# Kernel optimization log

Measured on AMD Instinct MI355X. Metric: run time of the kernel, lower is better.

## Reference

```python
import jax, jax.numpy as jnp
import numpy as np

IN_FEATURES = 256
OUT_FEATURES = 256
INTERNAL = (IN_FEATURES + OUT_FEATURES) // 2  # trajectron AdditiveAttention default


def setup_inputs() -> dict:
    key = jax.random.key(0)
    k1, k2, k3, k4, k5 = jax.random.split(key, 5)
    B, TH, TQ = 32, 256, 64
    inputs = jax.random.normal(k1, (B, TH, IN_FEATURES), dtype=jnp.float32)
    state = jax.random.normal(k2, (B, TQ, OUT_FEATURES), dtype=jnp.float32)
    # Linear weights (no bias), Kaiming-ish scale
    w1 = jax.random.normal(k3, (INTERNAL, IN_FEATURES), dtype=jnp.float32) / np.sqrt(IN_FEATURES)
    w2 = jax.random.normal(k4, (INTERNAL, OUT_FEATURES), dtype=jnp.float32) / np.sqrt(OUT_FEATURES)
    v = jax.random.normal(k5, (INTERNAL,), dtype=jnp.float32) / np.sqrt(INTERNAL)
    return {"inputs": inputs, "state": state, "w1": w1, "w2": w2, "v": v, "batch_size": B}


def reference(inputs, state, w1, w2, v, batch_size):
    # history annotations: (B, Th, Din); future annotations (queries): (B, Tq, Dout)
    keys = inputs.reshape(batch_size, -1, IN_FEATURES)
    queries = state.reshape(batch_size, -1, OUT_FEATURES)
    # Additive (Bahdanau) attention: score = v . tanh(W1 k + W2 q)
    k_proj = jnp.einsum('bti,di->btd', keys, w1)       # (B, Th, D)
    q_proj = jnp.einsum('bqo,do->bqd', queries, w2)    # (B, Tq, D)
    scores = jnp.einsum('d,bqtd->bqt', v, jnp.tanh(q_proj[:, :, None, :] + k_proj[:, None, :, :]))
    alpha = jax.nn.softmax(scores, axis=-1)            # softmax over history axis
    contexts = jnp.einsum('bqt,bti->bqi', alpha, keys)  # (B, Tq, Din)
    # reshape + dropout (eval mode / p effectively 0 -> identity)
    return contexts.reshape(-1, IN_FEATURES)
```

## Files before the change

kernel.cpp:

```cpp
#include <hip/hip_runtime.h>
#include <math.h>

#define BATCH 32
#define TH    256
#define TQn   64
#define DIN   256
#define DD    256
#define QT    4
#define E2C   2.885390081777927f
#define NL2E  -2.8853900817779268f

typedef __attribute__((ext_vector_type(8)))  short bf16x8;
typedef __attribute__((ext_vector_type(16))) float floatx16;
typedef __attribute__((ext_vector_type(4)))  float f32x4;
typedef __attribute__((ext_vector_type(2)))  float f32x2;

__device__ __forceinline__ float eclamp(float x) {
    return __builtin_amdgcn_exp2f(fminf(x * E2C, 15.f));
}

__device__ __forceinline__ f32x2 pk_fma_s(f32x2 a, f32x2 b, f32x2 c) {
    f32x2 d;
    asm("v_pk_fma_f32 %0, %1, %2, %3" : "=v"(d) : "s"(a), "v"(b), "v"(c));
    return d;
}
__device__ __forceinline__ f32x2 pk_mul_s(f32x2 a, f32x2 b) {
    f32x2 d;
    asm("v_pk_mul_f32 %0, %1, %2" : "=v"(d) : "s"(a), "v"(b));
    return d;
}
__device__ __forceinline__ f32x2 pk_mul_v(f32x2 a, f32x2 b) {
    f32x2 d;
    asm("v_pk_mul_f32 %0, %1, %2" : "=v"(d) : "v"(a), "v"(b));
    return d;
}

__device__ __forceinline__ unsigned cvt_pk_bf16(float x0, float x1) {
    unsigned r;
    asm("v_cvt_pk_bf16_f32 %0, %1, %2" : "=v"(r) : "v"(x0), "v"(x1));
    return r;
}
__device__ __forceinline__ void split2(float x0, float x1, unsigned& hi, unsigned& lo) {
    unsigned h = cvt_pk_bf16(x0, x1);
    float f0 = __uint_as_float(h << 16);
    float f1 = __uint_as_float(h & 0xFFFF0000u);
    hi = h;
    lo = cvt_pk_bf16(x0 - f0, x1 - f1);
}

__device__ __forceinline__ void split8(float4 f0, float4 f1, uint4& hi, uint4& lo) {
    split2(f0.x, f0.y, hi.x, lo.x);
    split2(f0.z, f0.w, hi.y, lo.y);
    split2(f1.x, f1.y, hi.z, lo.z);
    split2(f1.z, f1.w, hi.w, lo.w);
}

#define REG4  65
#define WOFF  (16 * REG4)
#define TSTR  68
__global__ __launch_bounds__(256, 4)
void proj_kernel(const float* __restrict__ keys,
                 const float* __restrict__ state,
                 const float* __restrict__ w1,
                 const float* __restrict__ w2,
                 const float* __restrict__ vvec,
                 float* __restrict__ ktp,
                 float* __restrict__ qpo,
                 float* __restrict__ vperm)
{
    __shared__ uint4 lds4[2 * 16 * REG4];

    const int bid = blockIdx.x;
    const int tid = threadIdx.x;

    const float* X;
    const float* W;
    int m0, n0;
    bool is_kp;
    if (bid < 512) {
        is_kp = true;
        m0 = (bid >> 2) * 64;
        n0 = (bid & 3) * 64;
        X = keys; W = w1;
    } else {
        is_kp = false;
        int lb = bid - 512;
        m0 = (lb >> 2) * 64;
        n0 = (lb & 3) * 64;
        X = state; W = w2;
    }

    const int w    = tid >> 6;
    const int l    = tid & 63;
    const int mt   = w >> 1;
    const int nt   = w & 1;
    const int srow = tid >> 3;
    const int kg   = tid & 7;
    const int s_s  = kg >> 1;
    const int lidx = (srow & 31) + 32 * (kg & 1);

    floatx16 acc = {};

    #pragma unroll
    for (int k0 = 0; k0 < DIN; k0 += 64) {
        #pragma unroll
        for (int hrow = 0; hrow < 2; hrow++) {
            int m = srow + hrow * 32;
            const float* px = X + (size_t)(m0 + m) * DIN + k0 + kg * 8;
            uint4 hi, lo;
            split8(*(const float4*)px, *(const float4*)(px + 4), hi, lo);
            int g = m >> 5;
            lds4[((0 * 2 + g) * 4 + s_s) * REG4 + lidx] = hi;
            lds4[((2 + g) * 4 + s_s) * REG4 + lidx] = lo;
            const float* pw = W + (size_t)(n0 + m) * DIN + k0 + kg * 8;
            split8(*(const float4*)pw, *(const float4*)(pw + 4), hi, lo);
            lds4[WOFF + ((0 * 2 + g) * 4 + s_s) * REG4 + lidx] = hi;
            lds4[WOFF + ((2 + g) * 4 + s_s) * REG4 + lidx] = lo;
        }
        __syncthreads();

        #pragma unroll
        for (int s = 0; s < 4; s++) {
            uint4 ahr = lds4[((0 * 2 + mt) * 4 + s) * REG4 + l];
            uint4 alr = lds4[((2 + mt) * 4 + s) * REG4 + l];
            uint4 bhr = lds4[WOFF + ((0 * 2 + nt) * 4 + s) * REG4 + l];
            uint4 blr = lds4[WOFF + ((2 + nt) * 4 + s) * REG4 + l];
            bf16x8 ah = __builtin_bit_cast(bf16x8, ahr);
            bf16x8 al = __builtin_bit_cast(bf16x8, alr);
            bf16x8 bh = __builtin_bit_cast(bf16x8, bhr);
            bf16x8 bl = __builtin_bit_cast(bf16x8, blr);
            acc = __builtin_amdgcn_mfma_f32_32x32x16_bf16(ah, bh, acc, 0, 0, 0);
            acc = __builtin_amdgcn_mfma_f32_32x32x16_bf16(al, bh, acc, 0, 0, 0);
            acc = __builtin_amdgcn_mfma_f32_32x32x16_bf16(ah, bl, acc, 0, 0, 0);
        }
        __syncthreads();
    }

    const int col = l & 31;
    const int hl  = l >> 5;
    if (is_kp) {
        float* sT = (float*)lds4;
        const int d_local = nt * 32 + col;
        #pragma unroll
        for (int r = 0; r < 16; r++) {
            int t_local = mt * 32 + 4 * hl + 8 * (r >> 2) + (r & 3);
            sT[t_local * TSTR + d_local] = eclamp(acc[r]);
        }
        __syncthreads();
        const int b  = m0 >> 8;
        const int t0 = m0 & 255;
        float4* dst4 = (float4*)ktp;
        #pragma unroll
        for (int p = 0; p < 4; p++) {
            int dp_local = w * 4 + p;
            float4 v4 = *(float4*)&sT[l * TSTR + dp_local * 4];
            float4 w4;
            w4.x = v4.x; w4.y = v4.z; w4.z = v4.y; w4.w = v4.w;
            dst4[(size_t)(b * 64 + (n0 >> 2) + dp_local) * 256 + t0 + l] = w4;
        }
    } else {
        const int d  = n0 + nt * 32 + col;
        const int dl = d & 3;
        const int dsd = (d & ~3) | ((dl & 1) << 1) | (dl >> 1);
        #pragma unroll
        for (int r = 0; r < 16; r++) {
            int row = (r & 3) + 8 * (r >> 2) + 4 * hl;
            qpo[(size_t)(m0 + mt * 32 + row) * DD + dsd] = eclamp(acc[r]);
        }
        if (bid == 512 && tid < 256) {
            int jl = tid & 3;
            vperm[tid] = vvec[(tid & ~3) | ((jl & 1) << 1) | (jl >> 1)];
        }
    }
}

__global__ __launch_bounds__(1024, 8)
void attn_kernel(const float* __restrict__ keys,
                 const float* __restrict__ vvec,
                 const float* __restrict__ ktp,
                 const float* __restrict__ qp,
                 float* __restrict__ out)
{
    __shared__ float s_part[4][QT][TH];
    __shared__ float s_alpha[QT][TH];
    __shared__ float s_rsum[QT];

    const int bid  = blockIdx.x;
    const int b    = bid & 31;
    const int q0   = (bid >> 5) * QT;
    const int tid  = threadIdx.x;
    const int t    = tid & 255;
    const int dgu  = __builtin_amdgcn_readfirstlane(tid >> 8);
    const int lane = tid & 63;
    const int wv   = tid >> 6;

    float acc[QT];
    #pragma unroll
    for (int q = 0; q < QT; q++) acc[q] = 0.f;

    const float4* kb4 = (const float4*)ktp + ((size_t)(b * 64 + dgu * 16) * 256 + t);
    const float* pqr0 = qp + (size_t)(b * TQn + q0 + 0) * DD + dgu * 64;
    const float* pqr1 = qp + (size_t)(b * TQn + q0 + 1) * DD + dgu * 64;
    const float* pqr2 = qp + (size_t)(b * TQn + q0 + 2) * DD + dgu * 64;
    const float* pqr3 = qp + (size_t)(b * TQn + q0 + 3) * DD + dgu * 64;
    const float* vvp  = vvec + dgu * 64;

    const f32x2 one2 = {1.f, 1.f};

    float4 kv0 = kb4[0 * 256], kv1 = kb4[1 * 256],
           kv2 = kb4[2 * 256], kv3 = kb4[3 * 256];

    #pragma unroll
    for (int c = 0; c < 4; c++) {
        float4 n0v, n1v, n2v, n3v;
        if (c < 3) {
            const float4* p = kb4 + (size_t)(c + 1) * 4 * 256;
            n0v = p[0 * 256]; n1v = p[1 * 256];
            n2v = p[2 * 256]; n3v = p[3 * 256];
        }
        #pragma unroll
        for (int u = 0; u < 4; u++) {
            const int dp = c * 4 + u;
            float4 kv = (u == 0) ? kv0 : (u == 1) ? kv1 : (u == 2) ? kv2 : kv3;
            f32x2 KA = {kv.x, kv.y};
            f32x2 KB = {kv.z, kv.w};
            f32x4 V4 = *(const f32x4*)(vvp + dp * 4);
            f32x2 VA = {V4[0], V4[1]};
            f32x2 VB = {V4[2], V4[3]};
            const float* pqr[QT] = {pqr0, pqr1, pqr2, pqr3};
            #pragma unroll
            for (int q = 0; q < QT; q++) {
                const float* pr = pqr[q];
                f32x4 P4 = *(const f32x4*)(pr + dp * 4);
                f32x2 PA = {P4[0], P4[1]};
                f32x2 PB = {P4[2], P4[3]};
                f32x2 A = pk_fma_s(PA, KA, one2);
                f32x2 B = pk_fma_s(PB, KB, one2);
                f32x2 D = pk_mul_v(A, B);
                f32x2 T = pk_mul_s(VA, B);
                f32x2 N = pk_fma_s(VB, A, T);
                float num = fmaf(N[1], D[0], N[0] * D[1]);
                float den = D[0] * D[1];
                acc[q] = fmaf(num, __builtin_amdgcn_rcpf(den), acc[q]);
            }
        }
        if (c < 3) { kv0 = n0v; kv1 = n1v; kv2 = n2v; kv3 = n3v; }
    }

    #pragma unroll
    for (int q = 0; q < QT; q++) s_part[dgu][q][t] = acc[q];
    __syncthreads();

    if (wv < QT) {
        const int q = wv;
        float p0 = s_part[0][q][lane]       + s_part[1][q][lane]
                 + s_part[2][q][lane]       + s_part[3][q][lane];
        float p1 = s_part[0][q][lane + 64]  + s_part[1][q][lane + 64]
                 + s_part[2][q][lane + 64]  + s_part[3][q][lane + 64];
        float p2 = s_part[0][q][lane + 128] + s_part[1][q][lane + 128]
                 + s_part[2][q][lane + 128] + s_part[3][q][lane + 128];
        float p3 = s_part[0][q][lane + 192] + s_part[1][q][lane + 192]
                 + s_part[2][q][lane + 192] + s_part[3][q][lane + 192];
        float e0 = __builtin_amdgcn_exp2f(p0 * NL2E);
        float e1 = __builtin_amdgcn_exp2f(p1 * NL2E);
        float e2 = __builtin_amdgcn_exp2f(p2 * NL2E);
        float e3 = __builtin_amdgcn_exp2f(p3 * NL2E);
        s_alpha[q][lane]       = e0;
        s_alpha[q][lane + 64]  = e1;
        s_alpha[q][lane + 128] = e2;
        s_alpha[q][lane + 192] = e3;
        float s = (e0 + e1) + (e2 + e3);
        #pragma unroll
        for (int off = 32; off >= 1; off >>= 1) s += __shfl_xor(s, off);
        if (lane == 0) s_rsum[q] = 1.f / s;
    }
    __syncthreads();

    {
        const int iqg = __builtin_amdgcn_readfirstlane((tid >> 6) & 3);
        const int il  = lane & 15;
        const int tl  = lane >> 4;
        const int iq  = iqg * 16 + il;

        f32x4 ctx4[QT] = {};
        const float* kp0 = keys + ((size_t)b * TH + dgu * 64 + tl) * DIN + iq * 4;

        #pragma unroll 4
        for (int step = 0; step < 16; step++) {
            f32x4 key4 = *(const f32x4*)(kp0 + (size_t)step * 4 * DIN);
            const int ta = dgu * 64 + step * 4 + tl;
            #pragma unroll
            for (int q = 0; q < QT; q++)
                ctx4[q] += key4 * s_alpha[q][ta];
        }

        #pragma unroll
        for (int q = 0; q < QT; q++) {
            #pragma unroll
            for (int k = 0; k < 4; k++) {
                ctx4[q][k] += __shfl_xor(ctx4[q][k], 16);
                ctx4[q][k] += __shfl_xor(ctx4[q][k], 32);
            }
        }
        if (tl == 0) {
            #pragma unroll
            for (int q = 0; q < QT; q++)
                *(f32x4*)&s_part[dgu][q][iq * 4] = ctx4[q];
        }
    }
    __syncthreads();

    if (tid < 256) {
        const int q = tid >> 6, iqf = tid & 63;
        f32x4 s = *(const f32x4*)&s_part[0][q][iqf * 4];
        s += *(const f32x4*)&s_part[1][q][iqf * 4];
        s += *(const f32x4*)&s_part[2][q][iqf * 4];
        s += *(const f32x4*)&s_part[3][q][iqf * 4];
        s *= s_rsum[q];
        *(f32x4*)&out[(size_t)(b * TQn + q0 + q) * DIN + iqf * 4] = s;
    }
}

extern "C" void kernel_launch(void* const* d_in, const int* in_sizes, int n_in,
                              void* d_out, int out_size, void* d_ws, size_t ws_size,
                              hipStream_t stream) {
    (void)in_sizes; (void)n_in; (void)out_size; (void)ws_size;
    const float* keys  = (const float*)d_in[0];
    const float* state = (const float*)d_in[1];
    const float* w1    = (const float*)d_in[2];
    const float* w2    = (const float*)d_in[3];
    const float* v     = (const float*)d_in[4];
    float* out = (float*)d_out;

    float* ktp = (float*)d_ws;
    float* qp  = ktp + (size_t)BATCH * DD * TH;
    float* vp  = qp + (size_t)BATCH * TQn * DD;

    hipLaunchKernelGGL(proj_kernel, dim3(640), dim3(256), 0, stream,
                       keys, state, w1, w2, v, ktp, qp, vp);
    hipLaunchKernelGGL(attn_kernel, dim3(BATCH * (TQn / QT)), dim3(1024), 0, stream,
                       keys, vp, ktp, qp, out);
}
```

Measured before the change: 101.7 us.

## Double queries per attention block, halve block size, transpose alpha for packed context FMA

```diff
diff --git a/kernel.cpp b/kernel.cpp
--- a/kernel.cpp
+++ b/kernel.cpp
@@ -6,9 +6,10 @@
 #define TQn   64
 #define DIN   256
 #define DD    256
-#define QT    4
+#define QT    8
 #define E2C   2.885390081777927f
 #define NL2E  -2.8853900817779268f
+#define ASTR  12
 
 typedef __attribute__((ext_vector_type(8)))  short bf16x8;
 typedef __attribute__((ext_vector_type(16))) float floatx16;
@@ -22,6 +23,11 @@
 __device__ __forceinline__ f32x2 pk_fma_s(f32x2 a, f32x2 b, f32x2 c) {
     f32x2 d;
     asm("v_pk_fma_f32 %0, %1, %2, %3" : "=v"(d) : "s"(a), "v"(b), "v"(c));
+    return d;
+}
+__device__ __forceinline__ f32x2 pk_fma_v(f32x2 a, f32x2 b, f32x2 c) {
+    f32x2 d;
+    asm("v_pk_fma_f32 %0, %1, %2, %3" : "=v"(d) : "v"(a), "v"(b), "v"(c));
     return d;
 }
 __device__ __forceinline__ f32x2 pk_mul_s(f32x2 a, f32x2 b) {
@@ -174,15 +180,15 @@
     }
 }
 
-__global__ __launch_bounds__(1024, 8)
+__global__ __launch_bounds__(512, 4)
 void attn_kernel(const float* __restrict__ keys,
                  const float* __restrict__ vvec,
                  const float* __restrict__ ktp,
                  const float* __restrict__ qp,
                  float* __restrict__ out)
 {
-    __shared__ float s_part[4][QT][TH];
-    __shared__ float s_alpha[QT][TH];
+    __shared__ float s_part[2][QT][TH];
+    __shared__ float s_alphaT[TH][ASTR];
     __shared__ float s_rsum[QT];
 
     const int bid  = blockIdx.x;
@@ -198,12 +204,9 @@
     #pragma unroll
     for (int q = 0; q < QT; q++) acc[q] = 0.f;
 
-    const float4* kb4 = (const float4*)ktp + ((size_t)(b * 64 + dgu * 16) * 256 + t);
-    const float* pqr0 = qp + (size_t)(b * TQn + q0 + 0) * DD + dgu * 64;
-    const float* pqr1 = qp + (size_t)(b * TQn + q0 + 1) * DD + dgu * 64;
-    const float* pqr2 = qp + (size_t)(b * TQn + q0 + 2) * DD + dgu * 64;
-    const float* pqr3 = qp + (size_t)(b * TQn + q0 + 3) * DD + dgu * 64;
-    const float* vvp  = vvec + dgu * 64;
+    const float4* kb4 = (const float4*)ktp + ((size_t)(b * 64 + dgu * 32) * 256 + t);
+    const float* pqb  = qp + (size_t)(b * TQn + q0) * DD + dgu * 128;
+    const float* vvp  = vvec + dgu * 128;
 
     const f32x2 one2 = {1.f, 1.f};
 
@@ -211,9 +214,9 @@
            kv2 = kb4[2 * 256], kv3 = kb4[3 * 256];
 
     #pragma unroll
-    for (int c = 0; c < 4; c++) {
+    for (int c = 0; c < 8; c++) {
         float4 n0v, n1v, n2v, n3v;
-        if (c < 3) {
+        if (c < 7) {
             const float4* p = kb4 + (size_t)(c + 1) * 4 * 256;
             n0v = p[0 * 256]; n1v = p[1 * 256];
             n2v = p[2 * 256]; n3v = p[3 * 256];
@@ -227,11 +230,9 @@
             f32x4 V4 = *(const f32x4*)(vvp + dp * 4);
             f32x2 VA = {V4[0], V4[1]};
             f32x2 VB = {V4[2], V4[3]};
-            const float* pqr[QT] = {pqr0, pqr1, pqr2, pqr3};
             #pragma unroll
             for (int q = 0; q < QT; q++) {
-                const float* pr = pqr[q];
-                f32x4 P4 = *(const f32x4*)(pr + dp * 4);
+                f32x4 P4 = *(const f32x4*)(pqb + q * DD + dp * 4);
                 f32x2 PA = {P4[0], P4[1]};
                 f32x2 PB = {P4[2], P4[3]};
                 f32x2 A = pk_fma_s(PA, KA, one2);
@@ -244,31 +245,27 @@
                 acc[q] = fmaf(num, __builtin_amdgcn_rcpf(den), acc[q]);
             }
         }
-        if (c < 3) { kv0 = n0v; kv1 = n1v; kv2 = n2v; kv3 = n3v; }
+        if (c < 7) { kv0 = n0v; kv1 = n1v; kv2 = n2v; kv3 = n3v; }
     }
 
     #pragma unroll
     for (int q = 0; q < QT; q++) s_part[dgu][q][t] = acc[q];
     __syncthreads();
 
-    if (wv < QT) {
+    {
         const int q = wv;
-        float p0 = s_part[0][q][lane]       + s_part[1][q][lane]
-                 + s_part[2][q][lane]       + s_part[3][q][lane];
-        float p1 = s_part[0][q][lane + 64]  + s_part[1][q][lane + 64]
-                 + s_part[2][q][lane + 64]  + s_part[3][q][lane + 64];
-        float p2 = s_part[0][q][lane + 128] + s_part[1][q][lane + 128]
-                 + s_part[2][q][lane + 128] + s_part[3][q][lane + 128];
-        float p3 = s_part[0][q][lane + 192] + s_part[1][q][lane + 192]
-                 + s_part[2][q][lane + 192] + s_part[3][q][lane + 192];
+        float p0 = s_part[0][q][lane]       + s_part[1][q][lane];
+        float p1 = s_part[0][q][lane + 64]  + s_part[1][q][lane + 64];
+        float p2 = s_part[0][q][lane + 128] + s_part[1][q][lane + 128];
+        float p3 = s_part[0][q][lane + 192] + s_part[1][q][lane + 192];
         float e0 = __builtin_amdgcn_exp2f(p0 * NL2E);
         float e1 = __builtin_amdgcn_exp2f(p1 * NL2E);
         float e2 = __builtin_amdgcn_exp2f(p2 * NL2E);
         float e3 = __builtin_amdgcn_exp2f(p3 * NL2E);
-        s_alpha[q][lane]       = e0;
-        s_alpha[q][lane + 64]  = e1;
-        s_alpha[q][lane + 128] = e2;
-        s_alpha[q][lane + 192] = e3;
+        s_alphaT[lane][q]       = e0;
+        s_alphaT[lane + 64][q]  = e1;
+        s_alphaT[lane + 128][q] = e2;
+        s_alphaT[lane + 192][q] = e3;
         float s = (e0 + e1) + (e2 + e3);
         #pragma unroll
         for (int off = 32; off >= 1; off >>= 1) s += __shfl_xor(s, off);
@@ -282,40 +279,54 @@
         const int tl  = lane >> 4;
         const int iq  = iqg * 16 + il;
 
-        f32x4 ctx4[QT] = {};
-        const float* kp0 = keys + ((size_t)b * TH + dgu * 64 + tl) * DIN + iq * 4;
+        f32x2 cq[4][4] = {};
+        const float* kp0 = keys + ((size_t)b * TH + dgu * 128 + tl) * DIN + iq * 4;
 
         #pragma unroll 4
-        for (int step = 0; step < 16; step++) {
+        for (int step = 0; step < 32; step++) {
             f32x4 key4 = *(const f32x4*)(kp0 + (size_t)step * 4 * DIN);
-            const int ta = dgu * 64 + step * 4 + tl;
+            const int ta = dgu * 128 + step * 4 + tl;
+            f32x4 a03 = *(const f32x4*)&s_alphaT[ta][0];
+            f32x4 a47 = *(const f32x4*)&s_alphaT[ta][4];
+            f32x2 ap[4] = {{a03[0], a03[1]}, {a03[2], a03[3]},
+                           {a47[0], a47[1]}, {a47[2], a47[3]}};
             #pragma unroll
-            for (int q = 0; q < QT; q++)
-                ctx4[q] += key4 * s_alpha[q][ta];
-        }
-
-        #pragma unroll
-        for (int q = 0; q < QT; q++) {
+            for (int i = 0; i < 4; i++) {
+                f32x2 kb = {key4[i], key4[i]};
+                #pragma unroll
+                for (int qp2 = 0; qp2 < 4; qp2++)
+                    cq[qp2][i] = pk_fma_v(ap[qp2], kb, cq[qp2][i]);
+            }
+        }
+
+        #pragma unroll
+        for (int qp2 = 0; qp2 < 4; qp2++) {
             #pragma unroll
-            for (int k = 0; k < 4; k++) {
-                ctx4[q][k] += __shfl_xor(ctx4[q][k], 16);
-                ctx4[q][k] += __shfl_xor(ctx4[q][k], 32);
+            for (int i = 0; i < 4; i++) {
+                #pragma unroll
+                for (int h = 0; h < 2; h++) {
+                    cq[qp2][i][h] += __shfl_xor(cq[qp2][i][h], 16);
+                    cq[qp2][i][h] += __shfl_xor(cq[qp2][i][h], 32);
+                }
             }
         }
         if (tl == 0) {
             #pragma unroll
-            for (int q = 0; q < QT; q++)
-                *(f32x4*)&s_part[dgu][q][iq * 4] = ctx4[q];
+            for (int qp2 = 0; qp2 < 4; qp2++) {
+                #pragma unroll
+                for (int i = 0; i < 4; i++) {
+                    s_part[dgu][2 * qp2 + 0][iq * 4 + i] = cq[qp2][i][0];
+                    s_part[dgu][2 * qp2 + 1][iq * 4 + i] = cq[qp2][i][1];
+                }
+            }
         }
     }
     __syncthreads();
 
-    if (tid < 256) {
+    {
         const int q = tid >> 6, iqf = tid & 63;
         f32x4 s = *(const f32x4*)&s_part[0][q][iqf * 4];
         s += *(const f32x4*)&s_part[1][q][iqf * 4];
-        s += *(const f32x4*)&s_part[2][q][iqf * 4];
-        s += *(const f32x4*)&s_part[3][q][iqf * 4];
         s *= s_rsum[q];
         *(f32x4*)&out[(size_t)(b * TQn + q0 + q) * DIN + iqf * 4] = s;
     }
@@ -338,6 +349,6 @@
 
     hipLaunchKernelGGL(proj_kernel, dim3(640), dim3(256), 0, stream,
                        keys, state, w1, w2, v, ktp, qp, vp);
-    hipLaunchKernelGGL(attn_kernel, dim3(BATCH * (TQn / QT)), dim3(1024), 0, stream,
+    hipLaunchKernelGGL(attn_kernel, dim3(BATCH * (TQn / QT)), dim3(512), 0, stream,
                        keys, vp, ktp, qp, out);
 }
```

Measured after the change: 102.6 us. About the same (+0.9%).
